# Optimization experiments

Measured on AMD Instinct MI355X. Metric: run time of the kernel, lower is better.

The kernel has to match this reference:

```python
import jax, jax.numpy as jnp
import numpy as np

N_NODES = 100000
N_HYPEREDGES = 30000
N_INC = 300000
IN_CH = 128
HID = 256
OUT_CH = 128
EPS = 1e-5


def setup_inputs() -> dict:
    key = jax.random.key(0)
    ks = jax.random.split(key, 14)
    x = jax.random.normal(ks[0], (N_NODES, IN_CH), jnp.float32)
    node_idx = jax.random.randint(ks[1], (N_INC,), 0, N_NODES)
    he_idx = jax.random.randint(ks[2], (N_INC,), 0, N_HYPEREDGES)
    edge = jnp.stack([node_idx, he_idx], axis=0)  # [2, N_INC]
    s1 = 1.0 / np.sqrt(IN_CH)
    s2 = 1.0 / np.sqrt(HID)
    return {
        "x": x,
        "edge": edge,
        "W1": jax.random.normal(ks[3], (IN_CH, HID), jnp.float32) * s1,
        "b1": jnp.zeros((HID,), jnp.float32),
        "g1": jnp.ones((HID,), jnp.float32),
        "be1": jnp.zeros((HID,), jnp.float32),
        "W2": jax.random.normal(ks[4], (HID, HID), jnp.float32) * s2,
        "b2": jnp.zeros((HID,), jnp.float32),
        "g2": jnp.ones((HID,), jnp.float32),
        "be2": jnp.zeros((HID,), jnp.float32),
        "W3": jax.random.normal(ks[5], (HID, OUT_CH), jnp.float32) * s2,
        "b3": jnp.zeros((OUT_CH,), jnp.float32),
    }


def _hconv(x, node_idx, he_idx, W, b):
    # PyG HypergraphConv (no attention, unit hyperedge weights):
    # X' = D^{-1} H B^{-1} H^T (X @ W) + b
    x = x @ W  # [N, F]
    ones = jnp.ones((node_idx.shape[0],), x.dtype)
    d = jax.ops.segment_sum(ones, node_idx, num_segments=N_NODES)       # node degree
    bd = jax.ops.segment_sum(ones, he_idx, num_segments=N_HYPEREDGES)  # hyperedge degree
    Dinv = jnp.where(d > 0, 1.0 / jnp.maximum(d, 1.0), 0.0)
    Binv = jnp.where(bd > 0, 1.0 / jnp.maximum(bd, 1.0), 0.0)
    # node -> hyperedge aggregation, scaled by B^{-1}
    he = jax.ops.segment_sum(x[node_idx], he_idx, num_segments=N_HYPEREDGES) * Binv[:, None]
    # hyperedge -> node aggregation, scaled by D^{-1}
    out = jax.ops.segment_sum(he[he_idx], node_idx, num_segments=N_NODES) * Dinv[:, None]
    return out + b


def _bn(x, g, be):
    # BatchNorm1d, training mode (batch statistics over nodes)
    m = x.mean(axis=0)
    v = x.var(axis=0)
    return (x - m) * jax.lax.rsqrt(v + EPS) * g + be


def reference(x, edge, W1, b1, g1, be1, W2, b2, g2, be2, W3, b3):
    node_idx = edge[0]
    he_idx = edge[1]
    h = _bn(jax.nn.relu(_hconv(x, node_idx, he_idx, W1, b1)), g1, be1)
    h = _bn(jax.nn.relu(_hconv(h, node_idx, he_idx, W2, b2)), g2, be2)
    h = jax.nn.relu(_hconv(h, node_idx, he_idx, W3, b3))
    return h
```

## Files before the change

### kernel.cpp

```cpp
#include <hip/hip_runtime.h>

#define N_NODES 100000
#define N_HE    30000
#define N_INC   300000
#define NTOT    (N_HE + N_NODES)
#define HEPAD   30080
#define NREP    16

typedef short  short8  __attribute__((ext_vector_type(8)));
typedef float  floatx4 __attribute__((ext_vector_type(4)));
typedef unsigned int uintx4 __attribute__((ext_vector_type(4)));

__device__ inline unsigned short f2bf(float f) {
  unsigned int u = __float_as_uint(f);
  u = (u + 0x7fff + ((u >> 16) & 1)) >> 16;
  return (unsigned short)u;
}
__device__ inline unsigned int pack2(float lo, float hi) {
  return (unsigned int)f2bf(lo) | ((unsigned int)f2bf(hi) << 16);
}
__device__ inline void acc8(uint4 rv, float* a) {
  unsigned int u;
  u = rv.x; a[0] += __uint_as_float(u << 16); a[1] += __uint_as_float(u & 0xffff0000u);
  u = rv.y; a[2] += __uint_as_float(u << 16); a[3] += __uint_as_float(u & 0xffff0000u);
  u = rv.z; a[4] += __uint_as_float(u << 16); a[5] += __uint_as_float(u & 0xffff0000u);
  u = rv.w; a[6] += __uint_as_float(u << 16); a[7] += __uint_as_float(u & 0xffff0000u);
}

struct R4 { uint4 r[4]; };
struct R8 { uint4 r[8]; };

__device__ inline void load4(const unsigned short* __restrict__ base, const int* e,
                             int F, int c0, R4& o) {
#pragma unroll
  for (int k = 0; k < 4; k++)
    o.r[k] = *(const uint4*)(base + (size_t)e[k] * F + c0);
}
__device__ inline void accm4(const R4& o, int d, float* a) {
  if (d > 0) acc8(o.r[0], a);
  if (d > 1) acc8(o.r[1], a);
  if (d > 2) acc8(o.r[2], a);
  if (d > 3) acc8(o.r[3], a);
}
__device__ inline void load8(const unsigned short* __restrict__ base, const int* e,
                             int F, int c0, R8& o) {
#pragma unroll
  for (int k = 0; k < 8; k++)
    o.r[k] = *(const uint4*)(base + (size_t)e[k] * F + c0);
}
__device__ inline void accm8(const R8& o, int d, float* a) {
  acc8(o.r[0], a);
  if (d > 1) acc8(o.r[1], a);
  if (d > 2) acc8(o.r[2], a);
  if (d > 3) acc8(o.r[3], a);
  if (d > 4) acc8(o.r[4], a);
  if (d > 5) acc8(o.r[5], a);
  if (d > 6) acc8(o.r[6], a);
  if (d > 7) acc8(o.r[7], a);
}

__device__ inline void gather8p(const unsigned short* __restrict__ base,
                                const int* __restrict__ idx, int beg, int end,
                                int F, int c0, float* a) {
  if (beg >= end) return;
  int e[8];
#pragma unroll
  for (int k = 0; k < 8; k++) e[k] = idx[min(beg + k, end - 1)];
  for (int j = beg; j < end; j += 8) {
    R8 r;
    load8(base, e, F, c0, r);
    int jn = j + 8;
    if (jn < end) {
#pragma unroll
      for (int k = 0; k < 8; k++) e[k] = idx[min(jn + k, end - 1)];
    }
    __builtin_amdgcn_sched_barrier(0);
    accm8(r, end - j, a);
  }
}


__global__ void count_convert(const int* __restrict__ nidx, const int* __restrict__ hidx,
                              int* __restrict__ cnt ,
                              const float* __restrict__ x, unsigned short* __restrict__ xb) {
  int i = blockIdx.x * 256 + threadIdx.x;
  if (i < N_INC) {
    atomicAdd(&cnt[N_HE + nidx[i]], 1);
    atomicAdd(&cnt[hidx[i]], 1);
  }
  if (i < N_NODES * 16) {
    const float4* p = (const float4*)x + (size_t)i * 2;
    float4 a = p[0], b = p[1];
    uint4 o;
    o.x = pack2(a.x, a.y); o.y = pack2(a.z, a.w);
    o.z = pack2(b.x, b.y); o.w = pack2(b.z, b.w);
    *(uint4*)(xb + (size_t)i * 8) = o;
  }
}

__global__ void scan1(const int* __restrict__ cnt, int* __restrict__ incl,
                      int* __restrict__ bsums, int n) {
  __shared__ int tmp[1024];
  int tid = threadIdx.x;
  int i = blockIdx.x * 1024 + tid;
  tmp[tid] = (i < n) ? cnt[i] : 0;
  __syncthreads();
  for (int off = 1; off < 1024; off <<= 1) {
    int t = (tid >= off) ? tmp[tid - off] : 0;
    __syncthreads();
    tmp[tid] += t;
    __syncthreads();
  }
  if (i < n) incl[i] = tmp[tid];
  if (tid == 1023) bsums[blockIdx.x] = tmp[1023];
}

__global__ void scan2(int* __restrict__ bsums, int nb) {
  __shared__ int tmp[128];
  int t = threadIdx.x;
  int my = (t < nb) ? bsums[t] : 0;
  tmp[t] = my;
  __syncthreads();
  for (int off = 1; off < 128; off <<= 1) {
    int v = (t >= off) ? tmp[t - off] : 0;
    __syncthreads();
    tmp[t] += v;
    __syncthreads();
  }
  if (t < nb) bsums[t] = tmp[t] - my;
}

__global__ void scan3c(const int* __restrict__ cnt, const int* __restrict__ incl,
                       const int* __restrict__ bsums,
                       int* __restrict__ he_ptr, int* __restrict__ he_fill,
                       int* __restrict__ node_ptr, int* __restrict__ node_fill) {
  int i = blockIdx.x * 1024 + threadIdx.x;
  if (i >= NTOT) return;
  int e = incl[i] - cnt[i] + bsums[blockIdx.x];
  if (i < N_HE) {
    he_ptr[i] = e;
    he_fill[i] = e;
    if (i == N_HE - 1) he_ptr[N_HE] = N_INC;
  } else {
    int v = e - N_INC;
    node_ptr[i - N_HE] = v;
    node_fill[i - N_HE] = v;
    if (i == NTOT - 1) node_ptr[N_NODES] = N_INC;
  }
}

__global__ void fill_kernel(const int* __restrict__ nidx, const int* __restrict__ hidx,
                            int* __restrict__ node_fill, int* __restrict__ he_fill,
                            int* __restrict__ node_hes, int* __restrict__ he_nodes) {
  int i = blockIdx.x * blockDim.x + threadIdx.x;
  if (i < N_INC) {
    int nn = nidx[i], hh = hidx[i];
    int p1 = atomicAdd(&node_fill[nn], 1);
    node_hes[p1] = hh;
    int p2 = atomicAdd(&he_fill[hh], 1);
    he_nodes[p2] = nn;
  }
}


__global__ __launch_bounds__(256) void fold_w(
    const float* __restrict__ W, const float* __restrict__ gsum,
    const float* __restrict__ gss, const float* __restrict__ g,
    const float* __restrict__ be, unsigned short* __restrict__ WT,
    float* __restrict__ cvec, int K, int N, float invN) {
  int n = blockIdx.y * 256 + threadIdx.x;
  if (n >= N) return;
  int k0 = blockIdx.x * 16;
  float c = 0.f;
  unsigned short loc[16];
#pragma unroll
  for (int i = 0; i < 16; i++) {
    int k = k0 + i;
    float w = W[(size_t)k * N + n];
    float s = 1.f, t = 0.f;
    if (gsum) {
      float ms = 0.f, vs = 0.f;
#pragma unroll
      for (int r = 0; r < NREP; r++) { ms += gsum[r * 256 + k]; vs += gss[r * 256 + k]; }
      float m = ms * invN;
      float v = vs * invN - m * m;
      s = g[k] * rsqrtf(v + 1e-5f);
      t = be[k] - m * s;
    }
    loc[i] = f2bf(w * s);
    c += t * w;
  }
  *(uint4*)(WT + (size_t)n * K + k0)     = *(const uint4*)&loc[0];
  *(uint4*)(WT + (size_t)n * K + k0 + 8) = *(const uint4*)&loc[8];
  atomicAdd(cvec + n, c);
}


__global__ __launch_bounds__(256) void gemm_mfma(
    const unsigned short* __restrict__ A, const unsigned short* __restrict__ BT,
    unsigned short* __restrict__ C, int K, int N) {
  __shared__ unsigned short As[128 * 32];
  __shared__ unsigned short Bs[128 * 32];
  const int tid  = threadIdx.x;
  const int w    = tid >> 6, lane = tid & 63;
  const int wm   = w & 1,  wn   = w >> 1;
  const int bm   = blockIdx.x * 128, bn = blockIdx.y * 128;
  const int quad = lane >> 4, r16 = lane & 15;

  floatx4 acc[4][4] = {};

  const int srow = (lane >> 2);
  const int scol = (lane & 3) * 8;

  for (int kb = 0; kb < K; kb += 32) {
#pragma unroll
    for (int i = 0; i < 2; i++) {
      const int row = (w * 2 + i) * 16 + srow;
      const unsigned short* ga = A  + (size_t)(bm + row) * K + kb + scol;
      const unsigned short* gb = BT + (size_t)(bn + row) * K + kb + scol;
      __builtin_amdgcn_global_load_lds(
          (const __attribute__((address_space(1))) void*)ga,
          (__attribute__((address_space(3))) void*)(&As[(w * 2 + i) * 512]), 16, 0, 0);
      __builtin_amdgcn_global_load_lds(
          (const __attribute__((address_space(1))) void*)gb,
          (__attribute__((address_space(3))) void*)(&Bs[(w * 2 + i) * 512]), 16, 0, 0);
    }
    __syncthreads();
    short8 af[4], bfr[4];
#pragma unroll
    for (int t = 0; t < 4; t++) {
      af[t]  = *(const short8*)&As[(wm * 64 + t * 16 + r16) * 32 + quad * 8];
      bfr[t] = *(const short8*)&Bs[(wn * 64 + t * 16 + r16) * 32 + quad * 8];
    }
#pragma unroll
    for (int mi = 0; mi < 4; mi++)
#pragma unroll
      for (int ni = 0; ni < 4; ni++)
        acc[mi][ni] = __builtin_amdgcn_mfma_f32_16x16x32_bf16(af[mi], bfr[ni], acc[mi][ni], 0, 0, 0);
    __syncthreads();
  }
#pragma unroll
  for (int mi = 0; mi < 4; mi++)
#pragma unroll
    for (int ni = 0; ni < 4; ni++)
#pragma unroll
      for (int rr = 0; rr < 4; rr++) {
        int gm = bm + wm * 64 + mi * 16 + quad * 4 + rr;
        int gn = bn + wn * 64 + ni * 16 + r16;
        C[(size_t)gm * N + gn] = f2bf(acc[mi][ni][rr]);
      }
}


__global__ __launch_bounds__(256, 4) void agg_he(
    const unsigned short* __restrict__ src, const int* __restrict__ ptr,
    const int* __restrict__ idx, unsigned short* __restrict__ dst,
    int F, int shift, int nSeg) {
  int seg = blockIdx.x * (256 >> shift) + (threadIdx.x >> shift);
  if (seg >= nSeg) return;
  int l = threadIdx.x & ((1 << shift) - 1);
  int c0 = l * 8;
  int beg = ptr[seg], end = ptr[seg + 1];
  float a[8] = {};
  gather8p(src, idx, beg, end, F, c0, a);
  float inv = (end > beg) ? 1.0f / (float)(end - beg) : 0.0f;
  uint4 o;
  o.x = pack2(a[0] * inv, a[1] * inv);
  o.y = pack2(a[2] * inv, a[3] * inv);
  o.z = pack2(a[4] * inv, a[5] * inv);
  o.w = pack2(a[6] * inv, a[7] * inv);
  *(uint4*)(dst + (size_t)seg * F + c0) = o;
}

__global__ __launch_bounds__(256, 4) void node_agg_bn(
    const unsigned short* __restrict__ he, const int* __restrict__ nptr,
    const int* __restrict__ nhes, const float* __restrict__ b,
    const float* __restrict__ cvec, unsigned short* __restrict__ dst,
    float* __restrict__ gsum, float* __restrict__ gss) {
  const int F = 256;
  const int bid = blockIdx.x;
  const int qi = (bid & 7) >> 1;
  const int xb = (bid >> 3) * 2 + (bid & 1);
  const int grp = threadIdx.x >> 3;
  const int l   = threadIdx.x & 7;
  const int c0  = qi * 64 + l * 8;
  float bb[8], cc[8];
#pragma unroll
  for (int j = 0; j < 8; j++) { bb[j] = b[c0 + j]; cc[j] = cvec[c0 + j]; }
  const int base_n = xb * 128 + grp * 4;
  int begs[4], ends[4];
#pragma unroll
  for (int i = 0; i < 4; i++) {
    int n = base_n + i;
    begs[i] = (n < N_NODES) ? nptr[n] : 0;
    ends[i] = (n < N_NODES) ? nptr[n + 1] : 0;
  }
  int e[4][4];
#pragma unroll
  for (int i = 0; i < 4; i++) {
#pragma unroll
    for (int k = 0; k < 4; k++)
      e[i][k] = (begs[i] < ends[i]) ? nhes[min(begs[i] + k, ends[i] - 1)] : 0;
  }
  R4 r0, r1, r2, r3;
  load4(he, e[0], F, c0, r0);
  load4(he, e[1], F, c0, r1);
  load4(he, e[2], F, c0, r2);
  load4(he, e[3], F, c0, r3);
  __builtin_amdgcn_sched_barrier(0);
  float sb[8] = {}, ssb[8] = {};
#pragma unroll
  for (int t = 0; t < 4; t++) {
    const int d = ends[t] - begs[t];
    float a[8] = {};
    const R4& rr = (t == 0) ? r0 : (t == 1) ? r1 : (t == 2) ? r2 : r3;
    accm4(rr, d, a);
    for (int j = begs[t] + 4; j < ends[t]; j += 4) {
      int et[4];
#pragma unroll
      for (int k = 0; k < 4; k++) et[k] = nhes[min(j + k, ends[t] - 1)];
      R4 tt; load4(he, et, F, c0, tt);
      accm4(tt, ends[t] - j, a);
    }
    const int n = base_n + t;
    if (n < N_NODES) {
      float inv  = (d > 0) ? 1.0f / (float)d : 0.0f;
      float cmul = (d > 0) ? 1.0f : 0.0f;
      float o[8];
#pragma unroll
      for (int j = 0; j < 8; j++) {
        o[j] = fmaxf(fmaf(a[j], inv, bb[j] + cmul * cc[j]), 0.f);
        sb[j] += o[j]; ssb[j] += o[j] * o[j];
      }
      uintx4 ov;
      ov.x = pack2(o[0], o[1]); ov.y = pack2(o[2], o[3]);
      ov.z = pack2(o[4], o[5]); ov.w = pack2(o[6], o[7]);
      __builtin_nontemporal_store(ov, (uintx4*)(dst + (size_t)n * F + c0));
    }
  }
  __shared__ float Ls[32][64];
  __shared__ float Lss[32][64];
#pragma unroll
  for (int j = 0; j < 8; j++) { Ls[grp][l * 8 + j] = sb[j]; Lss[grp][l * 8 + j] = ssb[j]; }
  __syncthreads();
  if (threadIdx.x < 64) {
    int c = threadIdx.x;
    float a1 = 0.f, a2 = 0.f;
#pragma unroll
    for (int h = 0; h < 32; h++) { a1 += Ls[h][c]; a2 += Lss[h][c]; }
    const int rep = xb & (NREP - 1);
    atomicAdd(gsum + rep * 256 + qi * 64 + c, a1);
    atomicAdd(gss  + rep * 256 + qi * 64 + c, a2);
  }
}

__global__ __launch_bounds__(256, 4) void agg_out(
    const unsigned short* __restrict__ he, const int* __restrict__ nptr,
    const int* __restrict__ nhes, const float* __restrict__ b,
    const float* __restrict__ cvec, float* __restrict__ out) {
  const int F = 128;
  const int bid = blockIdx.x;
  const int hi = (bid & 7) >> 2;
  const int xb = (bid >> 3) * 4 + (bid & 3);
  const int grp = threadIdx.x >> 3;
  const int l   = threadIdx.x & 7;
  const int c0  = hi * 64 + l * 8;
  float bb[8], cc[8];
#pragma unroll
  for (int j = 0; j < 8; j++) { bb[j] = b[c0 + j]; cc[j] = cvec[c0 + j]; }
  const int base_n = xb * 128 + grp * 4;
  int begs[4], ends[4];
#pragma unroll
  for (int i = 0; i < 4; i++) {
    int n = base_n + i;
    begs[i] = (n < N_NODES) ? nptr[n] : 0;
    ends[i] = (n < N_NODES) ? nptr[n + 1] : 0;
  }
  int e[4][4];
#pragma unroll
  for (int i = 0; i < 4; i++) {
#pragma unroll
    for (int k = 0; k < 4; k++)
      e[i][k] = (begs[i] < ends[i]) ? nhes[min(begs[i] + k, ends[i] - 1)] : 0;
  }
  R4 r0, r1, r2, r3;
  load4(he, e[0], F, c0, r0);
  load4(he, e[1], F, c0, r1);
  load4(he, e[2], F, c0, r2);
  load4(he, e[3], F, c0, r3);
  __builtin_amdgcn_sched_barrier(0);
#pragma unroll
  for (int t = 0; t < 4; t++) {
    const int d = ends[t] - begs[t];
    float a[8] = {};
    const R4& rr = (t == 0) ? r0 : (t == 1) ? r1 : (t == 2) ? r2 : r3;
    accm4(rr, d, a);
    for (int j = begs[t] + 4; j < ends[t]; j += 4) {
      int et[4];
#pragma unroll
      for (int k = 0; k < 4; k++) et[k] = nhes[min(j + k, ends[t] - 1)];
      R4 tt; load4(he, et, F, c0, tt);
      accm4(tt, ends[t] - j, a);
    }
    const int n = base_n + t;
    if (n < N_NODES) {
      float inv  = (d > 0) ? 1.0f / (float)d : 0.0f;
      float cmul = (d > 0) ? 1.0f : 0.0f;
      floatx4 o0, o1;
#pragma unroll
      for (int j = 0; j < 4; j++)
        o0[j] = fmaxf(fmaf(a[j], inv, bb[j] + cmul * cc[j]), 0.f);
#pragma unroll
      for (int j = 0; j < 4; j++)
        o1[j] = fmaxf(fmaf(a[4 + j], inv, bb[4 + j] + cmul * cc[4 + j]), 0.f);
      float* dp = out + (size_t)n * F + c0;
      __builtin_nontemporal_store(o0, (floatx4*)dp);
      __builtin_nontemporal_store(o1, (floatx4*)(dp + 4));
    }
  }
}


extern "C" void kernel_launch(void* const* d_in, const int* in_sizes, int n_in,
                              void* d_out, int out_size, void* d_ws, size_t ws_size,
                              hipStream_t stream) {
  const float* x    = (const float*)d_in[0];
  const int*   edge = (const int*)d_in[1];
  const int*   nidx = edge;
  const int*   hidx = edge + N_INC;
  const float* W1  = (const float*)d_in[2];
  const float* b1  = (const float*)d_in[3];
  const float* g1  = (const float*)d_in[4];
  const float* be1 = (const float*)d_in[5];
  const float* W2  = (const float*)d_in[6];
  const float* b2  = (const float*)d_in[7];
  const float* g2  = (const float*)d_in[8];
  const float* be2 = (const float*)d_in[9];
  const float* W3  = (const float*)d_in[10];
  const float* b3  = (const float*)d_in[11];
  float* out = (float*)d_out;

  char* ws = (char*)d_ws;
  size_t off = 0;
  auto alloc = [&](size_t bytes) -> void* {
    void* p = ws + off;
    off = (off + bytes + 255) & ~(size_t)255;
    return p;
  };
  unsigned short* Xb   = (unsigned short*)alloc((size_t)N_NODES * 128 * 2);
  unsigned short* Bb   = (unsigned short*)alloc((size_t)N_NODES * 256 * 2);
  unsigned short* Hraw = (unsigned short*)alloc((size_t)HEPAD * 256 * 2);
  unsigned short* HEb  = (unsigned short*)alloc((size_t)HEPAD * 256 * 2);
  unsigned short* W1T  = (unsigned short*)alloc((size_t)256 * 128 * 2);
  unsigned short* W2T  = (unsigned short*)alloc((size_t)256 * 256 * 2);
  unsigned short* W3T  = (unsigned short*)alloc((size_t)128 * 256 * 2);
  size_t zero_begin = off;
  int* cnt = (int*)alloc((size_t)NTOT * 4);
  float* gsum1 = (float*)alloc((size_t)NREP * 256 * 4);
  float* gss1  = (float*)alloc((size_t)NREP * 256 * 4);
  float* gsum2 = (float*)alloc((size_t)NREP * 256 * 4);
  float* gss2  = (float*)alloc((size_t)NREP * 256 * 4);
  float* c1 = (float*)alloc(1024);
  float* c2 = (float*)alloc(1024);
  float* c3 = (float*)alloc(1024);
  size_t zero_end = off;
  int* he_ptr    = (int*)alloc((size_t)(N_HE + 1) * 4);
  int* node_ptr  = (int*)alloc((size_t)(N_NODES + 1) * 4);
  int* he_fill   = (int*)alloc((size_t)N_HE * 4);
  int* node_fill = (int*)alloc((size_t)N_NODES * 4);
  int* he_nodes  = (int*)alloc((size_t)N_INC * 4);
  int* node_hes  = (int*)alloc((size_t)N_INC * 4);
  int* incl      = (int*)alloc((size_t)NTOT * 4);
  int* bsums     = (int*)alloc(512);

  hipMemsetAsync((void*)(ws + zero_begin), 0, zero_end - zero_begin, stream);

  count_convert<<<(N_NODES * 16 + 255) / 256, 256, 0, stream>>>(nidx, hidx, cnt, x, Xb);
  {
    int nb = (NTOT + 1023) / 1024;
    scan1<<<nb, 1024, 0, stream>>>(cnt, incl, bsums, NTOT);
    scan2<<<1, 128, 0, stream>>>(bsums, nb);
    scan3c<<<nb, 1024, 0, stream>>>(cnt, incl, bsums, he_ptr, he_fill, node_ptr, node_fill);
  }
  fill_kernel<<<(N_INC + 255) / 256, 256, 0, stream>>>(nidx, hidx, node_fill, he_fill,
                                                       node_hes, he_nodes);

  { dim3 g(128 / 16, 1);
    fold_w<<<g, 256, 0, stream>>>(W1, nullptr, nullptr, nullptr, nullptr, W1T, c1, 128, 256, 0.f); }

  const int MBHE = HEPAD / 128;
  const int QB = (N_NODES + 127) / 128;
  const int GRID_NA = 8 * ((QB + 1) / 2);
  const int GRID_AO = 8 * ((QB + 3) / 4);
  const float invN = 1.0f / (float)N_NODES;

  agg_he<<<(N_HE + 15) / 16, 256, 0, stream>>>(Xb, he_ptr, he_nodes, Hraw, 128, 4, N_HE);
  { dim3 g(MBHE, 2); gemm_mfma<<<g, 256, 0, stream>>>(Hraw, W1T, HEb, 128, 256); }
  node_agg_bn<<<GRID_NA, 256, 0, stream>>>(HEb, node_ptr, node_hes, b1, c1,
                                           Bb, gsum1, gss1);

  { dim3 g(256 / 16, 1);
    fold_w<<<g, 256, 0, stream>>>(W2, gsum1, gss1, g1, be1, W2T, c2, 256, 256, invN); }
  agg_he<<<(N_HE + 7) / 8, 256, 0, stream>>>(Bb, he_ptr, he_nodes, Hraw, 256, 5, N_HE);
  { dim3 g(MBHE, 2); gemm_mfma<<<g, 256, 0, stream>>>(Hraw, W2T, HEb, 256, 256); }
  node_agg_bn<<<GRID_NA, 256, 0, stream>>>(HEb, node_ptr, node_hes, b2, c2,
                                           Bb, gsum2, gss2);

  { dim3 g(256 / 16, 1);
    fold_w<<<g, 256, 0, stream>>>(W3, gsum2, gss2, g2, be2, W3T, c3, 256, 128, invN); }
  agg_he<<<(N_HE + 7) / 8, 256, 0, stream>>>(Bb, he_ptr, he_nodes, Hraw, 256, 5, N_HE);
  { dim3 g(MBHE, 1); gemm_mfma<<<g, 256, 0, stream>>>(Hraw, W3T, HEb, 256, 128); }
  agg_out<<<GRID_AO, 256, 0, stream>>>(HEb, node_ptr, node_hes, b3, c3, out);
}
```

Measured before the change: 402.4 us.

## Fold W1 conversion into count kernel and overlap BN weight folding on side stream

The standalone W1 transpose/convert launch is merged into count_convert as 8 extra blocks, and c1 is left at its zeroed value because there is no BN shift for layer 1. The fold_w launches for layers 2 and 3 now run on a second stream, synchronized with events, so they overlap with agg_he on the main stream. The aim is to cut launch count and hide the small fold kernels behind aggregation. The cost is event and cross-stream synchronization overhead, plus static stream state that persists across calls.

```diff
diff --git a/kernel.cpp b/kernel.cpp
--- a/kernel.cpp
+++ b/kernel.cpp
@@ -82,8 +82,21 @@
 
 __global__ void count_convert(const int* __restrict__ nidx, const int* __restrict__ hidx,
                               int* __restrict__ cnt ,
-                              const float* __restrict__ x, unsigned short* __restrict__ xb) {
-  int i = blockIdx.x * 256 + threadIdx.x;
+                              const float* __restrict__ x, unsigned short* __restrict__ xb,
+                              const float* __restrict__ W1, unsigned short* __restrict__ W1T,
+                              int nconv) {
+  int bid = blockIdx.x;
+  if (bid >= nconv) {
+    int k0 = (bid - nconv) * 16;
+    int n = threadIdx.x;
+    unsigned short loc[16];
+#pragma unroll
+    for (int i = 0; i < 16; i++) loc[i] = f2bf(W1[(size_t)(k0 + i) * 256 + n]);
+    *(uint4*)(W1T + (size_t)n * 128 + k0)     = *(const uint4*)&loc[0];
+    *(uint4*)(W1T + (size_t)n * 128 + k0 + 8) = *(const uint4*)&loc[8];
+    return;
+  }
+  int i = bid * 256 + threadIdx.x;
   if (i < N_INC) {
     atomicAdd(&cnt[N_HE + nidx[i]], 1);
     atomicAdd(&cnt[hidx[i]], 1);
@@ -177,16 +190,13 @@
   for (int i = 0; i < 16; i++) {
     int k = k0 + i;
     float w = W[(size_t)k * N + n];
-    float s = 1.f, t = 0.f;
-    if (gsum) {
-      float ms = 0.f, vs = 0.f;
-#pragma unroll
-      for (int r = 0; r < NREP; r++) { ms += gsum[r * 256 + k]; vs += gss[r * 256 + k]; }
-      float m = ms * invN;
-      float v = vs * invN - m * m;
-      s = g[k] * rsqrtf(v + 1e-5f);
-      t = be[k] - m * s;
-    }
+    float ms = 0.f, vs = 0.f;
+#pragma unroll
+    for (int r = 0; r < NREP; r++) { ms += gsum[r * 256 + k]; vs += gss[r * 256 + k]; }
+    float m = ms * invN;
+    float v = vs * invN - m * m;
+    float s = g[k] * rsqrtf(v + 1e-5f);
+    float t = be[k] - m * s;
     loc[i] = f2bf(w * s);
     c += t * w;
   }
@@ -439,6 +449,16 @@
   const float* W3  = (const float*)d_in[10];
   const float* b3  = (const float*)d_in[11];
   float* out = (float*)d_out;
+
+  static hipStream_t s2 = nullptr;
+  static hipEvent_t evF2 = nullptr, evJ2 = nullptr, evF3 = nullptr, evJ3 = nullptr;
+  if (s2 == nullptr) {
+    (void)hipStreamCreateWithFlags(&s2, hipStreamNonBlocking);
+    (void)hipEventCreateWithFlags(&evF2, hipEventDisableTiming);
+    (void)hipEventCreateWithFlags(&evJ2, hipEventDisableTiming);
+    (void)hipEventCreateWithFlags(&evF3, hipEventDisableTiming);
+    (void)hipEventCreateWithFlags(&evJ3, hipEventDisableTiming);
+  }
 
   char* ws = (char*)d_ws;
   size_t off = 0;
@@ -475,7 +495,8 @@
 
   hipMemsetAsync((void*)(ws + zero_begin), 0, zero_end - zero_begin, stream);
 
-  count_convert<<<(N_NODES * 16 + 255) / 256, 256, 0, stream>>>(nidx, hidx, cnt, x, Xb);
+  const int NCONV = (N_NODES * 16) / 256;
+  count_convert<<<NCONV + 8, 256, 0, stream>>>(nidx, hidx, cnt, x, Xb, W1, W1T, NCONV);
   {
     int nb = (NTOT + 1023) / 1024;
     scan1<<<nb, 1024, 0, stream>>>(cnt, incl, bsums, NTOT);
@@ -485,9 +506,6 @@
   fill_kernel<<<(N_INC + 255) / 256, 256, 0, stream>>>(nidx, hidx, node_fill, he_fill,
                                                        node_hes, he_nodes);
 
-  { dim3 g(128 / 16, 1);
-    fold_w<<<g, 256, 0, stream>>>(W1, nullptr, nullptr, nullptr, nullptr, W1T, c1, 128, 256, 0.f); }
-
   const int MBHE = HEPAD / 128;
   const int QB = (N_NODES + 127) / 128;
   const int GRID_NA = 8 * ((QB + 1) / 2);
@@ -499,16 +517,24 @@
   node_agg_bn<<<GRID_NA, 256, 0, stream>>>(HEb, node_ptr, node_hes, b1, c1,
                                            Bb, gsum1, gss1);
 
+  (void)hipEventRecord(evF2, stream);
+  (void)hipStreamWaitEvent(s2, evF2, 0);
   { dim3 g(256 / 16, 1);
-    fold_w<<<g, 256, 0, stream>>>(W2, gsum1, gss1, g1, be1, W2T, c2, 256, 256, invN); }
+    fold_w<<<g, 256, 0, s2>>>(W2, gsum1, gss1, g1, be1, W2T, c2, 256, 256, invN); }
   agg_he<<<(N_HE + 7) / 8, 256, 0, stream>>>(Bb, he_ptr, he_nodes, Hraw, 256, 5, N_HE);
+  (void)hipEventRecord(evJ2, s2);
+  (void)hipStreamWaitEvent(stream, evJ2, 0);
   { dim3 g(MBHE, 2); gemm_mfma<<<g, 256, 0, stream>>>(Hraw, W2T, HEb, 256, 256); }
   node_agg_bn<<<GRID_NA, 256, 0, stream>>>(HEb, node_ptr, node_hes, b2, c2,
                                            Bb, gsum2, gss2);
 
+  (void)hipEventRecord(evF3, stream);
+  (void)hipStreamWaitEvent(s2, evF3, 0);
   { dim3 g(256 / 16, 1);
-    fold_w<<<g, 256, 0, stream>>>(W3, gsum2, gss2, g2, be2, W3T, c3, 256, 128, invN); }
+    fold_w<<<g, 256, 0, s2>>>(W3, gsum2, gss2, g2, be2, W3T, c3, 256, 128, invN); }
   agg_he<<<(N_HE + 7) / 8, 256, 0, stream>>>(Bb, he_ptr, he_nodes, Hraw, 256, 5, N_HE);
+  (void)hipEventRecord(evJ3, s2);
+  (void)hipStreamWaitEvent(stream, evJ3, 0);
   { dim3 g(MBHE, 1); gemm_mfma<<<g, 256, 0, stream>>>(Hraw, W3T, HEb, 256, 128); }
   agg_out<<<GRID_AO, 256, 0, stream>>>(HEb, node_ptr, node_hes, b3, c3, out);
 }
```

Result: slower. 435.3 us (+8.2%).
